# Optimization experiments

Measured on AMD Instinct MI355X. Metric: run time of the kernel, lower is better.

Reference implementation:

```python
import jax, jax.numpy as jnp
import numpy as np

NUM_VARS = 64
EDGE_TYPES = 4
HID = 128
IN = 32
BATCH = 64
SKIP_FIRST = True


def setup_inputs() -> dict:
    key = jax.random.key(0)
    ks = jax.random.split(key, 16)
    adj = np.ones((NUM_VARS, NUM_VARS)) - np.eye(NUM_VARS)
    send, recv = np.where(adj)  # [N*(N-1)] each
    E = send.shape[0]
    s = 0.05
    return {
        'inputs': jax.random.normal(ks[0], (BATCH, NUM_VARS, IN), jnp.float32),
        'edges': jax.random.uniform(ks[1], (BATCH, E, EDGE_TYPES), dtype=jnp.float32),
        'msg_fc1_w': jax.random.normal(ks[2], (EDGE_TYPES, HID, 2 * IN), jnp.float32) * s,
        'msg_fc1_b': jax.random.normal(ks[3], (EDGE_TYPES, HID), jnp.float32) * s,
        'msg_fc2_w': jax.random.normal(ks[4], (EDGE_TYPES, HID, HID), jnp.float32) * s,
        'msg_fc2_b': jax.random.normal(ks[5], (EDGE_TYPES, HID), jnp.float32) * s,
        'out_fc1_w': jax.random.normal(ks[6], (HID, IN + HID), jnp.float32) * s,
        'out_fc1_b': jax.random.normal(ks[7], (HID,), jnp.float32) * s,
        'out_fc2_w': jax.random.normal(ks[8], (HID, HID), jnp.float32) * s,
        'out_fc2_b': jax.random.normal(ks[9], (HID,), jnp.float32) * s,
        'mu_w': jax.random.normal(ks[10], (IN, HID), jnp.float32) * s,
        'mu_b': jax.random.normal(ks[11], (IN,), jnp.float32) * s,
        'logstd_w': jax.random.normal(ks[12], (IN, HID), jnp.float32) * s,
        'logstd_b': jax.random.normal(ks[13], (IN,), jnp.float32) * s,
        'send_edges': jnp.asarray(send, jnp.int32),
        'recv_edges': jnp.asarray(recv, jnp.int32),
    }


def reference(inputs, edges, msg_fc1_w, msg_fc1_b, msg_fc2_w, msg_fc2_b,
              out_fc1_w, out_fc1_b, out_fc2_w, out_fc2_b,
              mu_w, mu_b, logstd_w, logstd_b, send_edges, recv_edges):
    # gather receiver/sender node features per edge: [B, E, 2*D]
    receivers = inputs[:, recv_edges, :]
    senders = inputs[:, send_edges, :]
    pre_msg = jnp.concatenate([receivers, senders], axis=-1)
    B, E, _ = pre_msg.shape
    all_msgs = jnp.zeros((B, E, HID), pre_msg.dtype)
    start = 1 if SKIP_FIRST else 0
    for i in range(start, EDGE_TYPES):  # small fixed loop over structurally distinct MLPs
        m = jax.nn.relu(jnp.einsum('bej,hj->beh', pre_msg, msg_fc1_w[i]) + msg_fc1_b[i])
        m = jax.nn.relu(jnp.einsum('beh,oh->beo', m, msg_fc2_w[i]) + msg_fc2_b[i])
        all_msgs = all_msgs + m * edges[:, :, i:i + 1]
    # scatter-add messages to receiver nodes (replaces dense one-hot matmul)
    agg_msgs = jnp.zeros((B, NUM_VARS, HID), all_msgs.dtype).at[:, recv_edges, :].add(all_msgs)
    aug_inputs = jnp.concatenate([inputs, agg_msgs], axis=-1)
    pred = jax.nn.relu(aug_inputs @ out_fc1_w.T + out_fc1_b)
    pred = jax.nn.relu(pred @ out_fc2_w.T + out_fc2_b)
    mu = pred @ mu_w.T + mu_b
    log_std = jnp.clip(pred @ logstd_w.T + logstd_b, -3.0, 1.0)
    std = jnp.exp(log_std)  # eval mode: std_gating = 0, noise suppressed
    pred_out = mu  # mu + 0 * noise * std
    return inputs + pred_out
```

## Files before the change

kernel.cpp:

```cpp
#include <hip/hip_runtime.h>
#include <hip/hip_bf16.h>
#include <hip/hip_fp16.h>

#define B_ 64
#define V_ 64
#define E_ 4032
#define HID_ 128
#define IN_ 32
#define BV_ (B_ * V_)

typedef __attribute__((ext_vector_type(8))) _Float16 f16x8;
typedef __attribute__((ext_vector_type(4))) float f32x4;

__global__ void __launch_bounds__(256) prep_all(
    const float* __restrict__ x, const float* __restrict__ w1,
    const float* __restrict__ b1, const float* __restrict__ w2,
    const float* __restrict__ edges, const float* __restrict__ fc1w,
    const float* __restrict__ fc2w, const float* __restrict__ muw,
    _Float16* __restrict__ h1r, _Float16* __restrict__ h1s,
    _Float16* __restrict__ w2f, _Float16* __restrict__ fc1f,
    _Float16* __restrict__ fc2f, _Float16* __restrict__ muf,
    _Float16* __restrict__ xh, float* __restrict__ ewT) {
  const int bid = blockIdx.x, t = threadIdx.x;

  if (bid < 256) {
    __shared__ float xs[16][IN_];
    for (int i = t; i < 16 * IN_; i += 256) xs[i >> 5][i & 31] = x[bid * 16 * IN_ + i];
    __syncthreads();
    const int h = t & 127, half_ = t >> 7;
#pragma unroll
    for (int tt = 0; tt < 3; ++tt) {
      const float* wrow = w1 + ((size_t)((tt + 1) * HID_ + h)) * (2 * IN_) + half_ * IN_;
      float4 w[8];
#pragma unroll
      for (int j = 0; j < 8; ++j) w[j] = ((const float4*)wrow)[j];
      const float bias = half_ ? 0.f : b1[(tt + 1) * HID_ + h];
      _Float16* dst = (half_ ? h1s : h1r) + ((size_t)tt * BV_ + bid * 16) * HID_ + h;
#pragma unroll
      for (int n = 0; n < 16; ++n) {
        float acc = bias;
#pragma unroll
        for (int j = 0; j < 8; ++j)
          acc += w[j].x * xs[n][4 * j] + w[j].y * xs[n][4 * j + 1] +
                 w[j].z * xs[n][4 * j + 2] + w[j].w * xs[n][4 * j + 3];
        dst[n * HID_] = (_Float16)acc;
      }
    }
    return;
  }
  if (bid < 448) {
    const int i = (bid - 256) * 256 + t;
    const int e = i & 7, lane = (i >> 3) & 63, ks = (i >> 9) & 3;
    const int nt = (i >> 11) & 1, w = (i >> 12) & 3, tt = i >> 14;
    const int o = w * 32 + nt * 16 + (lane & 15);
    const int k = ks * 32 + (lane >> 4) * 8 + e;
    w2f[i] = (_Float16)w2[((size_t)((tt + 1) * HID_ + o)) * HID_ + k];
    return;
  }
  if (bid < 608) {
    int i = (bid - 448) * 256 + t;
    if (i < 20480) {
      const int e = i & 7, lane = (i >> 3) & 63, rest = i >> 9;
      const int ks = rest % 5, ntg = rest / 5;
      const int o = ntg * 16 + (lane & 15);
      const int k = ks * 32 + (lane >> 4) * 8 + e;
      fc1f[i] = (_Float16)fc1w[(size_t)o * (IN_ + HID_) + k];
      return;
    }
    i -= 20480;
    if (i < 16384) {
      const int e = i & 7, lane = (i >> 3) & 63, rest = i >> 9;
      const int ks = rest & 3, ntg = rest >> 2;
      const int o = ntg * 16 + (lane & 15);
      const int k = ks * 32 + (lane >> 4) * 8 + e;
      fc2f[i] = (_Float16)fc2w[(size_t)o * HID_ + k];
      return;
    }
    i -= 16384;
    {
      const int e = i & 7, lane = (i >> 3) & 63, rest = i >> 9;
      const int ks = rest & 3, ntg = rest >> 2;
      const int o = ntg * 16 + (lane & 15);
      const int k = ks * 32 + (lane >> 4) * 8 + e;
      muf[i] = (_Float16)muw[(size_t)o * HID_ + k];
      return;
    }
  }
  if (bid < 736) {
    const int i4 = ((bid - 608) * 256 + t) * 4;
    float4 v4 = *(const float4*)(x + i4);
    _Float16 o[4] = {(_Float16)v4.x, (_Float16)v4.y, (_Float16)v4.z, (_Float16)v4.w};
    *(uint2*)(xh + i4) = *(const uint2*)o;
    return;
  }
  {
    const int g = bid - 736;
    if (t < 192) {
      const int b = g >> 6, v = g & 63;
      const int tt = t >> 6, r = t & 63;
      float val = 0.f;
      if (r < 63) {
        const int u = (r < v) ? r : r + 1;
        const int vv = (v > u) ? v - 1 : v;
        val = edges[((size_t)b * E_ + u * 63 + vv) * 4 + tt + 1];
      }
      ewT[(size_t)g * 192 + t] = val;
    }
    return;
  }
}

__global__ void __launch_bounds__(256)
edge_mfma(const float* __restrict__ b2, const _Float16* __restrict__ h1r,
          const _Float16* __restrict__ h1s, const _Float16* __restrict__ w2f,
          const float* __restrict__ ewT, _Float16* __restrict__ aggh) {
  const int bid = blockIdx.x;
  const int nb = (bid & 7) * 512 + (bid >> 3);
  const int b = nb >> 6, v = nb & 63;
  const int t = threadIdx.x;
  const int nh = t >> 6, lane = t & 63;
  const int l15 = lane & 15, lg = lane >> 4;

  __shared__ __align__(16) _Float16 hsl[64 * HID_];

  float acc[4][2][4];
#pragma unroll
  for (int mt = 0; mt < 4; ++mt)
#pragma unroll
    for (int nt = 0; nt < 2; ++nt)
#pragma unroll
      for (int r = 0; r < 4; ++r) acc[mt][nt][r] = 0.f;

  int urow[4];
#pragma unroll
  for (int mt = 0; mt < 4; ++mt) {
    const int r = mt * 16 + l15;
    int u = (r < v) ? r : r + 1;
    if (r == 63) u = v;
    urow[mt] = u;
  }

#pragma unroll
  for (int tt = 0; tt < 3; ++tt) {
    const char* hsb = (const char*)(h1s + ((size_t)(tt * B_ + b) * V_) * HID_);
#pragma unroll
    for (int q = 0; q < 4; ++q) {
      const int byteoff = q * 4096 + t * 16;
      const int row = (byteoff >> 8) & 7;
      f16x8 val = *(const f16x8*)(hsb + byteoff);
      *(f16x8*)((char*)hsl + (byteoff ^ (row << 4))) = val;
    }

    const _Float16* hrp = h1r + ((size_t)(tt * B_ + b) * V_ + v) * HID_;
    f16x8 hr[4];
#pragma unroll
    for (int ks = 0; ks < 4; ++ks) hr[ks] = *(const f16x8*)(hrp + ks * 32 + lg * 8);

    f16x8 bf[2][4];
    float b2r[2];
#pragma unroll
    for (int nt = 0; nt < 2; ++nt) {
#pragma unroll
      for (int ks = 0; ks < 4; ++ks)
        bf[nt][ks] = *(const f16x8*)(
            w2f + (size_t)(((((tt * 4 + nh) * 2 + nt) * 4 + ks) * 64 + lane)) * 8);
      b2r[nt] = b2[(tt + 1) * HID_ + nh * 32 + nt * 16 + l15];
    }
    __syncthreads();

#pragma unroll
    for (int mt = 0; mt < 4; ++mt) {
      const int u = urow[mt];
      const char* ubase = (const char*)hsl + u * 256;
      const int sw = (u & 7) << 4;
      f16x8 af[4];
#pragma unroll
      for (int ks = 0; ks < 4; ++ks) {
        f16x8 hs = *(const f16x8*)(ubase + ((ks * 64 + lg * 16) ^ sw));
        af[ks] = __builtin_elementwise_max(hr[ks] + hs, (f16x8)0);
      }
      const float4 ew4 =
          *(const float4*)(ewT + (size_t)nb * 192 + tt * 64 + mt * 16 + lg * 4);
#pragma unroll
      for (int nt = 0; nt < 2; ++nt) {
        f32x4 macc = {b2r[nt], b2r[nt], b2r[nt], b2r[nt]};
#pragma unroll
        for (int ks = 0; ks < 4; ++ks)
          macc = __builtin_amdgcn_mfma_f32_16x16x32_f16(af[ks], bf[nt][ks], macc, 0, 0, 0);
        acc[mt][nt][0] += fmaxf(macc[0], 0.f) * ew4.x;
        acc[mt][nt][1] += fmaxf(macc[1], 0.f) * ew4.y;
        acc[mt][nt][2] += fmaxf(macc[2], 0.f) * ew4.z;
        acc[mt][nt][3] += fmaxf(macc[3], 0.f) * ew4.w;
      }
    }
    __syncthreads();
  }

  float sv[2];
#pragma unroll
  for (int nt = 0; nt < 2; ++nt) {
    float s = 0.f;
#pragma unroll
    for (int mt = 0; mt < 4; ++mt)
#pragma unroll
      for (int r = 0; r < 4; ++r) s += acc[mt][nt][r];
    s += __shfl_xor(s, 16);
    s += __shfl_xor(s, 32);
    sv[nt] = s;
  }
  if (lane < 32)
    aggh[(size_t)nb * HID_ + nh * 32 + lane] = (_Float16)((lane < 16) ? sv[0] : sv[1]);
}

__global__ void __launch_bounds__(256)
out_mlp(const float* __restrict__ x, const _Float16* __restrict__ xh,
        const _Float16* __restrict__ aggh, const _Float16* __restrict__ fc1f,
        const float* __restrict__ fc1b, const _Float16* __restrict__ fc2f,
        const float* __restrict__ fc2b, const _Float16* __restrict__ muf,
        const float* __restrict__ mub, float* __restrict__ out) {
  const int t = threadIdx.x;
  const int lane = t & 63, l15 = lane & 15, lg = lane >> 4;
  const int w = t >> 6;
  const int nb = blockIdx.x * 16;

  __shared__ __align__(16) _Float16 p1h[16][136];
  __shared__ __align__(16) _Float16 p2h[16][136];

  const int arow = nb + l15;

  float4 acc1[2];
#pragma unroll
  for (int nt = 0; nt < 2; ++nt) {
    const float bias = fc1b[w * 32 + nt * 16 + l15];
    acc1[nt] = {bias, bias, bias, bias};
  }
#pragma unroll
  for (int ks = 0; ks < 5; ++ks) {
    f16x8 af = (ks == 0)
                   ? *(const f16x8*)(xh + (size_t)arow * IN_ + lg * 8)
                   : *(const f16x8*)(aggh + (size_t)arow * HID_ + (ks - 1) * 32 + lg * 8);
#pragma unroll
    for (int nt = 0; nt < 2; ++nt) {
      f16x8 bf = *(const f16x8*)(fc1f + (size_t)((((w * 2 + nt) * 5 + ks) * 64 + lane)) * 8);
      *(f32x4*)&acc1[nt] =
          __builtin_amdgcn_mfma_f32_16x16x32_f16(af, bf, *(f32x4*)&acc1[nt], 0, 0, 0);
    }
  }
#pragma unroll
  for (int nt = 0; nt < 2; ++nt) {
    const int col = w * 32 + nt * 16 + l15;
#pragma unroll
    for (int r = 0; r < 4; ++r)
      p1h[lg * 4 + r][col] = (_Float16)fmaxf(((const float*)&acc1[nt])[r], 0.f);
  }
  __syncthreads();

  float4 acc2[2];
#pragma unroll
  for (int nt = 0; nt < 2; ++nt) {
    const float bias = fc2b[w * 32 + nt * 16 + l15];
    acc2[nt] = {bias, bias, bias, bias};
  }
#pragma unroll
  for (int ks = 0; ks < 4; ++ks) {
    f16x8 af = *(const f16x8*)&p1h[l15][ks * 32 + lg * 8];
#pragma unroll
    for (int nt = 0; nt < 2; ++nt) {
      f16x8 bf = *(const f16x8*)(fc2f + (size_t)((((w * 2 + nt) * 4 + ks) * 64 + lane)) * 8);
      *(f32x4*)&acc2[nt] =
          __builtin_amdgcn_mfma_f32_16x16x32_f16(af, bf, *(f32x4*)&acc2[nt], 0, 0, 0);
    }
  }
#pragma unroll
  for (int nt = 0; nt < 2; ++nt) {
    const int col = w * 32 + nt * 16 + l15;
#pragma unroll
    for (int r = 0; r < 4; ++r)
      p2h[lg * 4 + r][col] = (_Float16)fmaxf(((const float*)&acc2[nt])[r], 0.f);
  }
  __syncthreads();

  if (w < 2) {
    const int col = w * 16 + l15;
    const float mb = mub[col];
    float4 acc3 = {mb, mb, mb, mb};
#pragma unroll
    for (int ks = 0; ks < 4; ++ks) {
      f16x8 af = *(const f16x8*)&p2h[l15][ks * 32 + lg * 8];
      f16x8 bf = *(const f16x8*)(muf + (size_t)(((w * 4 + ks) * 64 + lane)) * 8);
      *(f32x4*)&acc3 = __builtin_amdgcn_mfma_f32_16x16x32_f16(af, bf, *(f32x4*)&acc3, 0, 0, 0);
    }
#pragma unroll
    for (int r = 0; r < 4; ++r) {
      const int node = nb + lg * 4 + r;
      out[(size_t)node * IN_ + col] = x[(size_t)node * IN_ + col] + ((const float*)&acc3)[r];
    }
  }
}

extern "C" void kernel_launch(void* const* d_in, const int* in_sizes, int n_in,
                              void* d_out, int out_size, void* d_ws, size_t ws_size,
                              hipStream_t stream) {
  const float* x     = (const float*)d_in[0];
  const float* edges = (const float*)d_in[1];
  const float* w1    = (const float*)d_in[2];
  const float* b1    = (const float*)d_in[3];
  const float* w2    = (const float*)d_in[4];
  const float* b2    = (const float*)d_in[5];
  const float* fc1w  = (const float*)d_in[6];
  const float* fc1b  = (const float*)d_in[7];
  const float* fc2w  = (const float*)d_in[8];
  const float* fc2b  = (const float*)d_in[9];
  const float* muw   = (const float*)d_in[10];
  const float* mub   = (const float*)d_in[11];
  float* out = (float*)d_out;

  float* ewT    = (float*)d_ws;
  _Float16* h1r = (_Float16*)(ewT + (size_t)BV_ * 192);
  _Float16* h1s = h1r + (size_t)3 * BV_ * HID_;
  _Float16* w2f = h1s + (size_t)3 * BV_ * HID_;
  _Float16* fc1f = w2f + 49152;
  _Float16* fc2f = fc1f + 20480;
  _Float16* muf  = fc2f + 16384;
  _Float16* xh   = muf + 4096;
  _Float16* aggh = xh + (size_t)BV_ * IN_;

  prep_all<<<4832, 256, 0, stream>>>(x, w1, b1, w2, edges, fc1w, fc2w, muw,
                                     h1r, h1s, w2f, fc1f, fc2f, muf, xh, ewT);
  edge_mfma<<<BV_, 256, 0, stream>>>(b2, h1r, h1s, w2f, ewT, aggh);
  out_mlp<<<BV_ / 16, 256, 0, stream>>>(x, xh, aggh, fc1f, fc1b, fc2f, fc2b,
                                        muf, mub, out);
}
```

Baseline: 160.2 us.

## Retile edge MFMA waves to 2x2 layout and stage edge weights in LDS

The edge kernel's four waves move from one 32-column slice each to a 2x2 split of rows and columns, so each wave loads 64 output columns of w2 and handles 32 rows. This halves redundant A-fragment (hr+hs relu) construction per wave but doubles B-fragment registers, and adds an LDS cross-wave reduction plus an extra barrier. The prep kernel now uses smaller h1 blocks (4 nodes per block) for more parallelism. The edge-weight transpose now runs one block per batch that first loads that batch's edges into shared memory, replacing strided global gathers with LDS reads, at the cost of only 64 blocks each looping over 64 nodes.

After: 169.4 us. +5.7%, slower.

```diff
diff --git a/kernel.cpp b/kernel.cpp
--- a/kernel.cpp
+++ b/kernel.cpp
@@ -23,9 +23,9 @@
     _Float16* __restrict__ xh, float* __restrict__ ewT) {
   const int bid = blockIdx.x, t = threadIdx.x;
 
-  if (bid < 256) {
-    __shared__ float xs[16][IN_];
-    for (int i = t; i < 16 * IN_; i += 256) xs[i >> 5][i & 31] = x[bid * 16 * IN_ + i];
+  if (bid < 1024) {
+    __shared__ float xs[4][IN_];
+    if (t < 128) xs[t >> 5][t & 31] = x[bid * 128 + t];
     __syncthreads();
     const int h = t & 127, half_ = t >> 7;
 #pragma unroll
@@ -35,9 +35,9 @@
 #pragma unroll
       for (int j = 0; j < 8; ++j) w[j] = ((const float4*)wrow)[j];
       const float bias = half_ ? 0.f : b1[(tt + 1) * HID_ + h];
-      _Float16* dst = (half_ ? h1s : h1r) + ((size_t)tt * BV_ + bid * 16) * HID_ + h;
-#pragma unroll
-      for (int n = 0; n < 16; ++n) {
+      _Float16* dst = (half_ ? h1s : h1r) + ((size_t)tt * BV_ + bid * 4) * HID_ + h;
+#pragma unroll
+      for (int n = 0; n < 4; ++n) {
         float acc = bias;
 #pragma unroll
         for (int j = 0; j < 8; ++j)
@@ -48,17 +48,17 @@
     }
     return;
   }
-  if (bid < 448) {
-    const int i = (bid - 256) * 256 + t;
+  if (bid < 1216) {
+    const int i = (bid - 1024) * 256 + t;
     const int e = i & 7, lane = (i >> 3) & 63, ks = (i >> 9) & 3;
-    const int nt = (i >> 11) & 1, w = (i >> 12) & 3, tt = i >> 14;
-    const int o = w * 32 + nt * 16 + (lane & 15);
+    const int nt4 = (i >> 11) & 3, nh2 = (i >> 13) & 1, tt = i >> 14;
+    const int o = nh2 * 64 + nt4 * 16 + (lane & 15);
     const int k = ks * 32 + (lane >> 4) * 8 + e;
     w2f[i] = (_Float16)w2[((size_t)((tt + 1) * HID_ + o)) * HID_ + k];
     return;
   }
-  if (bid < 608) {
-    int i = (bid - 448) * 256 + t;
+  if (bid < 1376) {
+    int i = (bid - 1216) * 256 + t;
     if (i < 20480) {
       const int e = i & 7, lane = (i >> 3) & 63, rest = i >> 9;
       const int ks = rest % 5, ntg = rest / 5;
@@ -86,25 +86,31 @@
       return;
     }
   }
-  if (bid < 736) {
-    const int i4 = ((bid - 608) * 256 + t) * 4;
+  if (bid < 1504) {
+    const int i4 = ((bid - 1376) * 256 + t) * 4;
     float4 v4 = *(const float4*)(x + i4);
     _Float16 o[4] = {(_Float16)v4.x, (_Float16)v4.y, (_Float16)v4.z, (_Float16)v4.w};
     *(uint2*)(xh + i4) = *(const uint2*)o;
     return;
   }
   {
-    const int g = bid - 736;
-    if (t < 192) {
-      const int b = g >> 6, v = g & 63;
-      const int tt = t >> 6, r = t & 63;
-      float val = 0.f;
-      if (r < 63) {
-        const int u = (r < v) ? r : r + 1;
-        const int vv = (v > u) ? v - 1 : v;
-        val = edges[((size_t)b * E_ + u * 63 + vv) * 4 + tt + 1];
+    const int b = bid - 1504;
+    __shared__ float ed[E_ * 4];
+    for (int i = t; i < E_; i += 256) {
+      *(float4*)&ed[i * 4] = *(const float4*)(edges + ((size_t)b * E_ + i) * 4);
+    }
+    __syncthreads();
+    for (int v = 0; v < V_; ++v) {
+      if (t < 192) {
+        const int tt = t >> 6, r = t & 63;
+        float val = 0.f;
+        if (r < 63) {
+          const int u = (r < v) ? r : r + 1;
+          const int vv = (v > u) ? v - 1 : v;
+          val = ed[(u * 63 + vv) * 4 + tt + 1];
+        }
+        ewT[((size_t)(b * V_ + v)) * 192 + t] = val;
       }
-      ewT[(size_t)g * 192 + t] = val;
     }
     return;
   }
@@ -118,28 +124,31 @@
   const int nb = (bid & 7) * 512 + (bid >> 3);
   const int b = nb >> 6, v = nb & 63;
   const int t = threadIdx.x;
-  const int nh = t >> 6, lane = t & 63;
+  const int wave = t >> 6, lane = t & 63;
+  const int mh = wave & 1, nhh = wave >> 1;
   const int l15 = lane & 15, lg = lane >> 4;
 
   __shared__ __align__(16) _Float16 hsl[64 * HID_];
-
-  float acc[4][2][4];
-#pragma unroll
-  for (int mt = 0; mt < 4; ++mt)
-#pragma unroll
-    for (int nt = 0; nt < 2; ++nt)
-#pragma unroll
-      for (int r = 0; r < 4; ++r) acc[mt][nt][r] = 0.f;
-
-  int urow[4];
-#pragma unroll
-  for (int mt = 0; mt < 4; ++mt) {
-    const int r = mt * 16 + l15;
+  __shared__ float pshare[2][HID_];
+
+  float acc[2][4][4];
+#pragma unroll
+  for (int m = 0; m < 2; ++m)
+#pragma unroll
+    for (int nt = 0; nt < 4; ++nt)
+#pragma unroll
+      for (int r = 0; r < 4; ++r) acc[m][nt][r] = 0.f;
+
+  int urow[2];
+#pragma unroll
+  for (int m = 0; m < 2; ++m) {
+    const int r = mh * 32 + m * 16 + l15;
     int u = (r < v) ? r : r + 1;
     if (r == 63) u = v;
-    urow[mt] = u;
-  }
-
+    urow[m] = u;
+  }
+
+  float b2r[4];
 #pragma unroll
   for (int tt = 0; tt < 3; ++tt) {
     const char* hsb = (const char*)(h1s + ((size_t)(tt * B_ + b) * V_) * HID_);
@@ -156,21 +165,20 @@
 #pragma unroll
     for (int ks = 0; ks < 4; ++ks) hr[ks] = *(const f16x8*)(hrp + ks * 32 + lg * 8);
 
-    f16x8 bf[2][4];
-    float b2r[2];
-#pragma unroll
-    for (int nt = 0; nt < 2; ++nt) {
+    f16x8 bf[4][4];
+#pragma unroll
+    for (int nt = 0; nt < 4; ++nt) {
 #pragma unroll
       for (int ks = 0; ks < 4; ++ks)
         bf[nt][ks] = *(const f16x8*)(
-            w2f + (size_t)(((((tt * 4 + nh) * 2 + nt) * 4 + ks) * 64 + lane)) * 8);
-      b2r[nt] = b2[(tt + 1) * HID_ + nh * 32 + nt * 16 + l15];
+            w2f + (size_t)(((((tt * 2 + nhh) * 4 + nt) * 4 + ks) * 64 + lane)) * 8);
+      b2r[nt] = b2[(tt + 1) * HID_ + nhh * 64 + nt * 16 + l15];
     }
     __syncthreads();
 
 #pragma unroll
-    for (int mt = 0; mt < 4; ++mt) {
-      const int u = urow[mt];
+    for (int m = 0; m < 2; ++m) {
+      const int u = urow[m];
       const char* ubase = (const char*)hsl + u * 256;
       const int sw = (u & 7) << 4;
       f16x8 af[4];
@@ -179,37 +187,37 @@
         f16x8 hs = *(const f16x8*)(ubase + ((ks * 64 + lg * 16) ^ sw));
         af[ks] = __builtin_elementwise_max(hr[ks] + hs, (f16x8)0);
       }
-      const float4 ew4 =
-          *(const float4*)(ewT + (size_t)nb * 192 + tt * 64 + mt * 16 + lg * 4);
-#pragma unroll
-      for (int nt = 0; nt < 2; ++nt) {
+      const float4 ew4 = *(const float4*)(ewT + (size_t)nb * 192 + tt * 64 +
+                                          (mh * 2 + m) * 16 + lg * 4);
+#pragma unroll
+      for (int nt = 0; nt < 4; ++nt) {
         f32x4 macc = {b2r[nt], b2r[nt], b2r[nt], b2r[nt]};
 #pragma unroll
         for (int ks = 0; ks < 4; ++ks)
           macc = __builtin_amdgcn_mfma_f32_16x16x32_f16(af[ks], bf[nt][ks], macc, 0, 0, 0);
-        acc[mt][nt][0] += fmaxf(macc[0], 0.f) * ew4.x;
-        acc[mt][nt][1] += fmaxf(macc[1], 0.f) * ew4.y;
-        acc[mt][nt][2] += fmaxf(macc[2], 0.f) * ew4.z;
-        acc[mt][nt][3] += fmaxf(macc[3], 0.f) * ew4.w;
+        acc[m][nt][0] += fmaxf(macc[0], 0.f) * ew4.x;
+        acc[m][nt][1] += fmaxf(macc[1], 0.f) * ew4.y;
+        acc[m][nt][2] += fmaxf(macc[2], 0.f) * ew4.z;
+        acc[m][nt][3] += fmaxf(macc[3], 0.f) * ew4.w;
       }
     }
     __syncthreads();
   }
 
-  float sv[2];
-#pragma unroll
-  for (int nt = 0; nt < 2; ++nt) {
+#pragma unroll
+  for (int nt = 0; nt < 4; ++nt) {
     float s = 0.f;
 #pragma unroll
-    for (int mt = 0; mt < 4; ++mt)
-#pragma unroll
-      for (int r = 0; r < 4; ++r) s += acc[mt][nt][r];
+    for (int m = 0; m < 2; ++m)
+#pragma unroll
+      for (int r = 0; r < 4; ++r) s += acc[m][nt][r];
     s += __shfl_xor(s, 16);
     s += __shfl_xor(s, 32);
-    sv[nt] = s;
-  }
-  if (lane < 32)
-    aggh[(size_t)nb * HID_ + nh * 32 + lane] = (_Float16)((lane < 16) ? sv[0] : sv[1]);
+    if (lane < 16) pshare[mh][nhh * 64 + nt * 16 + l15] = s;
+  }
+  __syncthreads();
+  if (t < HID_)
+    aggh[(size_t)nb * HID_ + t] = (_Float16)(pshare[0][t] + pshare[1][t]);
 }
 
 __global__ void __launch_bounds__(256)
@@ -325,7 +333,7 @@
   _Float16* xh   = muf + 4096;
   _Float16* aggh = xh + (size_t)BV_ * IN_;
 
-  prep_all<<<4832, 256, 0, stream>>>(x, w1, b1, w2, edges, fc1w, fc2w, muw,
+  prep_all<<<1568, 256, 0, stream>>>(x, w1, b1, w2, edges, fc1w, fc2w, muw,
                                      h1r, h1s, w2f, fc1f, fc2f, muf, xh, ewT);
   edge_mfma<<<BV_, 256, 0, stream>>>(b2, h1r, h1s, w2f, ewT, aggh);
   out_mlp<<<BV_ / 16, 256, 0, stream>>>(x, xh, aggh, fc1f, fc1b, fc2f, fc2b,
```
